# Kernel tuning notes

Hardware: AMD Instinct MI355X
Metric: run time of the kernel (lower is better)

## Reference

```python
import jax, jax.numpy as jnp
import numpy as np

B = 16384      # batch (original code uses B=1; break generalized per-sample)
H = 1024       # MLP hidden width from MLP([2, 1024, 1])
NMAX = 10      # RModel nmax default


def _mlp(x, W1, b1, W2, b2):
    # Linear(2->H) + ELU, then Linear(H->1) (no final activation: act=None)
    h = jax.nn.elu(x @ W1.T + b1)
    return h @ W2.T + b2


def setup_inputs() -> dict:
    key = jax.random.key(0)
    ks = jax.random.split(key, 5)
    X = jax.random.normal(ks[0], (B, 1), dtype=jnp.float32)
    Y = jnp.zeros((B, 1), dtype=jnp.float32)
    # _init_layers: Linear weights ~ N(0, 0.5), biases = 0
    de_W1 = 0.5 * jax.random.normal(ks[1], (H, 2), dtype=jnp.float32)
    de_b1 = jnp.zeros((H,), dtype=jnp.float32)
    de_W2 = 0.5 * jax.random.normal(ks[2], (1, H), dtype=jnp.float32)
    de_b2 = jnp.zeros((1,), dtype=jnp.float32)
    val_W1 = 0.5 * jax.random.normal(ks[3], (H, 2), dtype=jnp.float32)
    val_b1 = jnp.zeros((H,), dtype=jnp.float32)
    val_W2 = 0.5 * jax.random.normal(ks[4], (1, H), dtype=jnp.float32)
    val_b2 = jnp.zeros((1,), dtype=jnp.float32)
    return {"X": X, "Y": Y,
            "de_W1": de_W1, "de_b1": de_b1, "de_W2": de_W2, "de_b2": de_b2,
            "val_W1": val_W1, "val_b1": val_b1, "val_W2": val_W2, "val_b2": val_b2}


def reference(X, Y, de_W1, de_b1, de_W2, de_b2, val_W1, val_b1, val_W2, val_b2):
    # xen/yen are identity (defaults)
    xsig = X
    v0 = _mlp(jnp.concatenate([xsig, Y], axis=1), val_W1, val_b1, val_W2, val_b2)
    done0 = jnp.zeros((X.shape[0], 1), dtype=bool)

    def step(carry, i):
        y_prev, v_prev, done = carry
        y_new = y_prev + _mlp(jnp.concatenate([xsig, y_prev], axis=1),
                              de_W1, de_b1, de_W2, de_b2)
        v_new = _mlp(jnp.concatenate([xsig, y_new], axis=1),
                     val_W1, val_b1, val_W2, val_b2)
        # samples that already broke keep (freeze) their last appended (Y, V)
        y = jnp.where(done, y_prev, y_new)
        v = jnp.where(done, v_prev, v_new)
        # break condition: i > 0 and V >= previous V (appended first, then break)
        done = done | ((i > 0) & (v_new >= v_prev))
        return (y, v, done), (y, v)

    _, (ys, vs) = jax.lax.scan(step, (Y, v0, done0), jnp.arange(NMAX))
    y_stack = jnp.concatenate([Y[None], ys], axis=0)   # [NMAX+1, B, 1]
    v_stack = jnp.concatenate([v0[None], vs], axis=0)  # [NMAX+1, B, 1]
    return (y_stack, v_stack)
```

## Files before the change

kernel.cpp:

```cpp
#include <hip/hip_runtime.h>

#define NMAX 10
#define KPL  16
#define L2E  1.4426950408889634f
#define LN2  0.6931471805599453f

typedef float f2 __attribute__((ext_vector_type(2)));

template<int CTRL, int RMASK, int BMASK>
__device__ __forceinline__ float dppmov(float v) {
    return __int_as_float(__builtin_amdgcn_update_dpp(
        0, __float_as_int(v), CTRL, RMASK, BMASK, true));
}
__device__ __forceinline__ float rdlane63(float v) {
    return __int_as_float(__builtin_amdgcn_readlane(__float_as_int(v), 63));
}

__device__ __forceinline__ void wred2(float& a, float& b) {
    a += dppmov<0xB1, 0xf, 0xf>(a);  b += dppmov<0xB1, 0xf, 0xf>(b);
    a += dppmov<0x4E, 0xf, 0xf>(a);  b += dppmov<0x4E, 0xf, 0xf>(b);
    a += dppmov<0x141,0xf, 0xf>(a);  b += dppmov<0x141,0xf, 0xf>(b);
    a += dppmov<0x140,0xf, 0xf>(a);  b += dppmov<0x140,0xf, 0xf>(b);
    a += dppmov<0x142,0xa, 0xf>(a);  b += dppmov<0x142,0xa, 0xf>(b);
    a += dppmov<0x143,0xc, 0xf>(a);  b += dppmov<0x143,0xc, 0xf>(b);
    a = rdlane63(a);                 b = rdlane63(b);
}

__device__ __forceinline__ void mlp_joint(
    const float4* __restrict__ wl,
    const f2 (&u)[KPL],
    float y, float dbias, float vbias, float& dout, float& vout)
{
    const f2 yv   = {y, y};
    const f2 l2e  = {L2E, L2E};
    const f2 nl2e = {-L2E, -L2E};
    f2 acc0 = {0.f, 0.f}, acc1 = {0.f, 0.f};
#pragma unroll
    for (int k = 0; k < KPL; k += 2) {
        const float4 wa = wl[k * 64];
        const float4 wb = wl[(k + 1) * 64];
        f2 wya = {wa.x, wa.y}, w2a = {wa.z, wa.w};
        f2 wyb = {wb.x, wb.y}, w2b = {wb.z, wb.w};
        f2 p0 = __builtin_elementwise_fma(wya, yv, u[k]);
        f2 p1 = __builtin_elementwise_fma(wyb, yv, u[k + 1]);
        f2 e0, e1;
        e0.x = __builtin_amdgcn_exp2f(p0.x);  e0.y = __builtin_amdgcn_exp2f(p0.y);
        e1.x = __builtin_amdgcn_exp2f(p1.x);  e1.y = __builtin_amdgcn_exp2f(p1.y);
        f2 z0 = __builtin_elementwise_fma(e0, l2e, nl2e);
        f2 z1 = __builtin_elementwise_fma(e1, l2e, nl2e);
        f2 m0, m1;
        m0.x = __builtin_amdgcn_fmed3f(p0.x, z0.x, 0.f);
        m0.y = __builtin_amdgcn_fmed3f(p0.y, z0.y, 0.f);
        m1.x = __builtin_amdgcn_fmed3f(p1.x, z1.x, 0.f);
        m1.y = __builtin_amdgcn_fmed3f(p1.y, z1.y, 0.f);
        acc0 = __builtin_elementwise_fma(w2a, m0, acc0);
        acc1 = __builtin_elementwise_fma(w2b, m1, acc1);
    }
    float a = acc0.x + acc1.x;
    float b = acc0.y + acc1.y;
    wred2(a, b);
    dout = a + dbias; vout = b + vbias;
}

__global__ __launch_bounds__(256) void rmodel_kernel(
    const float* __restrict__ X, const float* __restrict__ Y,
    const float* __restrict__ de_W1, const float* __restrict__ de_b1,
    const float* __restrict__ de_W2, const float* __restrict__ de_b2,
    const float* __restrict__ val_W1, const float* __restrict__ val_b1,
    const float* __restrict__ val_W2, const float* __restrict__ val_b2,
    float* __restrict__ out, int n)
{
    __shared__ float4 wlds[KPL * 64];

    const int tid  = threadIdx.x;
    const int wid  = tid >> 6;
    const int lane = tid & 63;
    const int b    = blockIdx.x * 4 + wid;

#pragma unroll
    for (int i = 0; i < 4; ++i) {
        const int h = tid + i * 256;
        float2 w1d = reinterpret_cast<const float2*>(de_W1)[h];
        float2 w1v = reinterpret_cast<const float2*>(val_W1)[h];
        wlds[h] = make_float4(w1d.y * L2E, w1v.y * L2E,
                              de_W2[h] * LN2, val_W2[h] * LN2);
    }
    __syncthreads();

    if (b >= n) return;

    f2 u[KPL];
    const float x  = X[b];
    const float y0 = Y[b];
#pragma unroll
    for (int k = 0; k < KPL; ++k) {
        const int h = k * 64 + lane;
        float2 w1d = reinterpret_cast<const float2*>(de_W1)[h];
        float2 w1v = reinterpret_cast<const float2*>(val_W1)[h];
        u[k] = (f2){fmaf(w1d.x, x, de_b1[h]) * L2E,
                    fmaf(w1v.x, x, val_b1[h]) * L2E};
    }
    const float db2 = de_b2[0];
    const float vb2 = val_b2[0];
    const float4* wl = &wlds[lane];

    float* __restrict__ yout = out;
    float* __restrict__ vout = out + (size_t)(NMAX + 1) * n;

    float d, v;
    mlp_joint(wl, u, y0, db2, vb2, d, v);
    if (lane == 0) { yout[b] = y0; vout[b] = v; }

    float y     = y0 + d;
    float vprev = v;
    float yfin  = y0, vfin = v;
    int   kend  = NMAX;

    float* yp = yout + b;
    float* vp = vout + b;
    for (int k = 1; k <= NMAX; ++k) {
        yp += n; vp += n;
        float dk, vk;
        mlp_joint(wl, u, y, db2, vb2, dk, vk);
        if (lane == 0) { *yp = y; *vp = vk; }
        yfin = y; vfin = vk;
        if (k >= 2 && vk >= vprev) { kend = k; break; }
        vprev = vk;
        y += dk;
    }

    const int r = kend + 1 + lane;
    if (r <= NMAX) {
        yout[(size_t)r * n + b] = yfin;
        vout[(size_t)r * n + b] = vfin;
    }
}

extern "C" void kernel_launch(void* const* d_in, const int* in_sizes, int n_in,
                              void* d_out, int out_size, void* d_ws, size_t ws_size,
                              hipStream_t stream) {
    const float* X      = (const float*)d_in[0];
    const float* Y      = (const float*)d_in[1];
    const float* de_W1  = (const float*)d_in[2];
    const float* de_b1  = (const float*)d_in[3];
    const float* de_W2  = (const float*)d_in[4];
    const float* de_b2  = (const float*)d_in[5];
    const float* val_W1 = (const float*)d_in[6];
    const float* val_b1 = (const float*)d_in[7];
    const float* val_W2 = (const float*)d_in[8];
    const float* val_b2 = (const float*)d_in[9];
    float* out = (float*)d_out;

    const int n = in_sizes[0];
    dim3 block(256);
    dim3 grid((n + 3) / 4);
    hipLaunchKernelGGL(rmodel_kernel, grid, block, 0, stream,
                       X, Y, de_W1, de_b1, de_W2, de_b2,
                       val_W1, val_b1, val_W2, val_b2, out, n);
}
```

Before: 65.90 us.

## Process two samples per wavefront to share LDS weight loads and reductions

Each wavefront now handles a pair of samples, computing both MLP evaluations in one pass so every LDS weight float4 load serves two samples and the DPP cross-lane reductions are batched four-wide. When one sample breaks early, the other continues alone through a single-sample fallback loop. This adds register pressure (two sets of 16 precomputed u values) and halves the grid, and the per-step cost follows the slower sample of each pair.

```diff
diff --git a/kernel.cpp b/kernel.cpp
--- a/kernel.cpp
+++ b/kernel.cpp
@@ -16,50 +16,91 @@
     return __int_as_float(__builtin_amdgcn_readlane(__float_as_int(v), 63));
 }
 
+#define WRED_STAGE(CTRL, RM) \
+    a += dppmov<CTRL, RM, 0xf>(a);  b += dppmov<CTRL, RM, 0xf>(b);
+
 __device__ __forceinline__ void wred2(float& a, float& b) {
-    a += dppmov<0xB1, 0xf, 0xf>(a);  b += dppmov<0xB1, 0xf, 0xf>(b);
-    a += dppmov<0x4E, 0xf, 0xf>(a);  b += dppmov<0x4E, 0xf, 0xf>(b);
-    a += dppmov<0x141,0xf, 0xf>(a);  b += dppmov<0x141,0xf, 0xf>(b);
-    a += dppmov<0x140,0xf, 0xf>(a);  b += dppmov<0x140,0xf, 0xf>(b);
-    a += dppmov<0x142,0xa, 0xf>(a);  b += dppmov<0x142,0xa, 0xf>(b);
-    a += dppmov<0x143,0xc, 0xf>(a);  b += dppmov<0x143,0xc, 0xf>(b);
-    a = rdlane63(a);                 b = rdlane63(b);
+    WRED_STAGE(0xB1, 0xf)
+    WRED_STAGE(0x4E, 0xf)
+    WRED_STAGE(0x141,0xf)
+    WRED_STAGE(0x140,0xf)
+    WRED_STAGE(0x142,0xa)
+    WRED_STAGE(0x143,0xc)
+    a = rdlane63(a);  b = rdlane63(b);
+}
+
+#define WRED4_STAGE(CTRL, RM) \
+    a += dppmov<CTRL, RM, 0xf>(a);  b += dppmov<CTRL, RM, 0xf>(b); \
+    c += dppmov<CTRL, RM, 0xf>(c);  d += dppmov<CTRL, RM, 0xf>(d);
+
+__device__ __forceinline__ void wred4(float& a, float& b, float& c, float& d) {
+    WRED4_STAGE(0xB1, 0xf)
+    WRED4_STAGE(0x4E, 0xf)
+    WRED4_STAGE(0x141,0xf)
+    WRED4_STAGE(0x140,0xf)
+    WRED4_STAGE(0x142,0xa)
+    WRED4_STAGE(0x143,0xc)
+    a = rdlane63(a);  b = rdlane63(b);  c = rdlane63(c);  d = rdlane63(d);
+}
+
+__device__ __forceinline__ void unit_step(const float4 w, const f2 u, const f2 yv, f2& acc) {
+    const f2 l2e  = {L2E, L2E};
+    const f2 nl2e = {-L2E, -L2E};
+    f2 wy = {w.x, w.y}, w2 = {w.z, w.w};
+    f2 p = __builtin_elementwise_fma(wy, yv, u);
+    f2 e;
+    e.x = __builtin_amdgcn_exp2f(p.x);  e.y = __builtin_amdgcn_exp2f(p.y);
+    f2 z = __builtin_elementwise_fma(e, l2e, nl2e);
+    f2 m;
+    m.x = __builtin_amdgcn_fmed3f(p.x, z.x, 0.f);
+    m.y = __builtin_amdgcn_fmed3f(p.y, z.y, 0.f);
+    acc = __builtin_elementwise_fma(w2, m, acc);
 }
 
 __device__ __forceinline__ void mlp_joint(
-    const float4* __restrict__ wl,
-    const f2 (&u)[KPL],
+    const float4* __restrict__ wl, const f2 (&u)[KPL],
     float y, float dbias, float vbias, float& dout, float& vout)
 {
-    const f2 yv   = {y, y};
-    const f2 l2e  = {L2E, L2E};
-    const f2 nl2e = {-L2E, -L2E};
+    const f2 yv = {y, y};
     f2 acc0 = {0.f, 0.f}, acc1 = {0.f, 0.f};
 #pragma unroll
     for (int k = 0; k < KPL; k += 2) {
         const float4 wa = wl[k * 64];
         const float4 wb = wl[(k + 1) * 64];
-        f2 wya = {wa.x, wa.y}, w2a = {wa.z, wa.w};
-        f2 wyb = {wb.x, wb.y}, w2b = {wb.z, wb.w};
-        f2 p0 = __builtin_elementwise_fma(wya, yv, u[k]);
-        f2 p1 = __builtin_elementwise_fma(wyb, yv, u[k + 1]);
-        f2 e0, e1;
-        e0.x = __builtin_amdgcn_exp2f(p0.x);  e0.y = __builtin_amdgcn_exp2f(p0.y);
-        e1.x = __builtin_amdgcn_exp2f(p1.x);  e1.y = __builtin_amdgcn_exp2f(p1.y);
-        f2 z0 = __builtin_elementwise_fma(e0, l2e, nl2e);
-        f2 z1 = __builtin_elementwise_fma(e1, l2e, nl2e);
-        f2 m0, m1;
-        m0.x = __builtin_amdgcn_fmed3f(p0.x, z0.x, 0.f);
-        m0.y = __builtin_amdgcn_fmed3f(p0.y, z0.y, 0.f);
-        m1.x = __builtin_amdgcn_fmed3f(p1.x, z1.x, 0.f);
-        m1.y = __builtin_amdgcn_fmed3f(p1.y, z1.y, 0.f);
-        acc0 = __builtin_elementwise_fma(w2a, m0, acc0);
-        acc1 = __builtin_elementwise_fma(w2b, m1, acc1);
+        unit_step(wa, u[k],     yv, acc0);
+        unit_step(wb, u[k + 1], yv, acc1);
     }
     float a = acc0.x + acc1.x;
     float b = acc0.y + acc1.y;
     wred2(a, b);
     dout = a + dbias; vout = b + vbias;
+}
+
+__device__ __forceinline__ void mlp_joint2(
+    const float4* __restrict__ wl,
+    const f2 (&uA)[KPL], const f2 (&uB)[KPL],
+    float yA, float yB, float dbias, float vbias,
+    float& dA, float& vA, float& dB, float& vB)
+{
+    const f2 yvA = {yA, yA}, yvB = {yB, yB};
+    f2 aA0 = {0.f, 0.f}, aA1 = {0.f, 0.f};
+    f2 aB0 = {0.f, 0.f}, aB1 = {0.f, 0.f};
+#pragma unroll
+    for (int k = 0; k < KPL; k += 2) {
+        const float4 wa = wl[k * 64];
+        const float4 wb = wl[(k + 1) * 64];
+        unit_step(wa, uA[k],     yvA, aA0);
+        unit_step(wa, uB[k],     yvB, aB0);
+        unit_step(wb, uA[k + 1], yvA, aA1);
+        unit_step(wb, uB[k + 1], yvB, aB1);
+    }
+    float a = aA0.x + aA1.x;
+    float b = aA0.y + aA1.y;
+    float c = aB0.x + aB1.x;
+    float d = aB0.y + aB1.y;
+    wred4(a, b, c, d);
+    dA = a + dbias; vA = b + vbias;
+    dB = c + dbias; vB = d + vbias;
 }
 
 __global__ __launch_bounds__(256) void rmodel_kernel(
@@ -75,7 +116,6 @@
     const int tid  = threadIdx.x;
     const int wid  = tid >> 6;
     const int lane = tid & 63;
-    const int b    = blockIdx.x * 4 + wid;
 
 #pragma unroll
     for (int i = 0; i < 4; ++i) {
@@ -87,18 +127,23 @@
     }
     __syncthreads();
 
-    if (b >= n) return;
-
-    f2 u[KPL];
-    const float x  = X[b];
-    const float y0 = Y[b];
+    const int p  = blockIdx.x * 4 + wid;
+    const int bA = 2 * p;
+    if (bA >= n) return;
+    const bool hasB = (bA + 1 < n);
+    const int bB = hasB ? bA + 1 : bA;
+
+    f2 uA[KPL], uB[KPL];
+    const float xA = X[bA], xB = X[bB];
+    const float y0A = Y[bA], y0B = Y[bB];
 #pragma unroll
     for (int k = 0; k < KPL; ++k) {
         const int h = k * 64 + lane;
         float2 w1d = reinterpret_cast<const float2*>(de_W1)[h];
         float2 w1v = reinterpret_cast<const float2*>(val_W1)[h];
-        u[k] = (f2){fmaf(w1d.x, x, de_b1[h]) * L2E,
-                    fmaf(w1v.x, x, val_b1[h]) * L2E};
+        const float bd = de_b1[h], bv = val_b1[h];
+        uA[k] = (f2){fmaf(w1d.x, xA, bd) * L2E, fmaf(w1v.x, xA, bv) * L2E};
+        uB[k] = (f2){fmaf(w1d.x, xB, bd) * L2E, fmaf(w1v.x, xB, bv) * L2E};
     }
     const float db2 = de_b2[0];
     const float vb2 = val_b2[0];
@@ -107,32 +152,71 @@
     float* __restrict__ yout = out;
     float* __restrict__ vout = out + (size_t)(NMAX + 1) * n;
 
-    float d, v;
-    mlp_joint(wl, u, y0, db2, vb2, d, v);
-    if (lane == 0) { yout[b] = y0; vout[b] = v; }
-
-    float y     = y0 + d;
-    float vprev = v;
-    float yfin  = y0, vfin = v;
-    int   kend  = NMAX;
-
-    float* yp = yout + b;
-    float* vp = vout + b;
-    for (int k = 1; k <= NMAX; ++k) {
-        yp += n; vp += n;
+    float dA, vA, dB, vB;
+    mlp_joint2(wl, uA, uB, y0A, y0B, db2, vb2, dA, vA, dB, vB);
+    if (lane == 0) {
+        yout[bA] = y0A; vout[bA] = vA;
+        if (hasB) { yout[bB] = y0B; vout[bB] = vB; }
+    }
+
+    float yA = y0A + dA, yB = y0B + dB;
+    float vpA = vA, vpB = vB;
+    float yfinA = y0A, vfinA = vA, yfinB = y0B, vfinB = vB;
+    int kendA = NMAX, kendB = NMAX;
+    bool actA = true, actB = hasB;
+    int k = 1;
+
+    while (k <= NMAX && actA && actB) {
+        float dkA, vkA, dkB, vkB;
+        mlp_joint2(wl, uA, uB, yA, yB, db2, vb2, dkA, vkA, dkB, vkB);
+        if (lane == 0) {
+            yout[(size_t)k * n + bA] = yA; vout[(size_t)k * n + bA] = vkA;
+            yout[(size_t)k * n + bB] = yB; vout[(size_t)k * n + bB] = vkB;
+        }
+        yfinA = yA; vfinA = vkA; yfinB = yB; vfinB = vkB;
+        const bool brkA = (k >= 2) && (vkA >= vpA);
+        const bool brkB = (k >= 2) && (vkB >= vpB);
+        vpA = vkA; vpB = vkB;
+        if (brkA) { kendA = k; actA = false; } else { yA += dkA; }
+        if (brkB) { kendB = k; actB = false; } else { yB += dkB; }
+        ++k;
+    }
+    while (k <= NMAX && actA) {
         float dk, vk;
-        mlp_joint(wl, u, y, db2, vb2, dk, vk);
-        if (lane == 0) { *yp = y; *vp = vk; }
-        yfin = y; vfin = vk;
-        if (k >= 2 && vk >= vprev) { kend = k; break; }
-        vprev = vk;
-        y += dk;
-    }
-
-    const int r = kend + 1 + lane;
-    if (r <= NMAX) {
-        yout[(size_t)r * n + b] = yfin;
-        vout[(size_t)r * n + b] = vfin;
+        mlp_joint(wl, uA, yA, db2, vb2, dk, vk);
+        if (lane == 0) {
+            yout[(size_t)k * n + bA] = yA; vout[(size_t)k * n + bA] = vk;
+        }
+        yfinA = yA; vfinA = vk;
+        const bool brk = (k >= 2) && (vk >= vpA);
+        vpA = vk;
+        if (brk) { kendA = k; actA = false; } else { yA += dk; }
+        ++k;
+    }
+    while (k <= NMAX && actB) {
+        float dk, vk;
+        mlp_joint(wl, uB, yB, db2, vb2, dk, vk);
+        if (lane == 0) {
+            yout[(size_t)k * n + bB] = yB; vout[(size_t)k * n + bB] = vk;
+        }
+        yfinB = yB; vfinB = vk;
+        const bool brk = (k >= 2) && (vk >= vpB);
+        vpB = vk;
+        if (brk) { kendB = k; actB = false; } else { yB += dk; }
+        ++k;
+    }
+
+    const int rA = kendA + 1 + lane;
+    if (rA <= NMAX) {
+        yout[(size_t)rA * n + bA] = yfinA;
+        vout[(size_t)rA * n + bA] = vfinA;
+    }
+    if (hasB) {
+        const int rB = kendB + 1 + lane;
+        if (rB <= NMAX) {
+            yout[(size_t)rB * n + bB] = yfinB;
+            vout[(size_t)rB * n + bB] = vfinB;
+        }
     }
 }
 
@@ -151,9 +235,10 @@
     const float* val_b2 = (const float*)d_in[9];
     float* out = (float*)d_out;
 
-    const int n = in_sizes[0];
+    const int n     = in_sizes[0];
+    const int pairs = (n + 1) / 2;
     dim3 block(256);
-    dim3 grid((n + 3) / 4);
+    dim3 grid((pairs + 3) / 4);
     hipLaunchKernelGGL(rmodel_kernel, grid, block, 0, stream,
                        X, Y, de_W1, de_b1, de_W2, de_b2,
                        val_W1, val_b1, val_W2, val_b2, out, n);
```

Result: no change. 65.34 us (-0.9%).

## Split joint de/val MLP evaluation to skip unused final de network pass

Applied to the files above, without the earlier changes.

Evaluates the value and delta MLPs separately instead of jointly, so the delta network is only computed when its output will be used (not on the breaking or last iteration). The weight layout in shared memory is reorganized so each float4 packs two hidden units of one network. This removes wasted exp/FMA work but halves per-call instruction-level parallelism and doubles the number of cross-lane reductions.

```diff
diff --git a/kernel.cpp b/kernel.cpp
--- a/kernel.cpp
+++ b/kernel.cpp
@@ -1,7 +1,7 @@
 #include <hip/hip_runtime.h>
 
 #define NMAX 10
-#define KPL  16
+#define NP   8
 #define L2E  1.4426950408889634f
 #define LN2  0.6931471805599453f
 
@@ -16,50 +16,45 @@
     return __int_as_float(__builtin_amdgcn_readlane(__float_as_int(v), 63));
 }
 
-__device__ __forceinline__ void wred2(float& a, float& b) {
-    a += dppmov<0xB1, 0xf, 0xf>(a);  b += dppmov<0xB1, 0xf, 0xf>(b);
-    a += dppmov<0x4E, 0xf, 0xf>(a);  b += dppmov<0x4E, 0xf, 0xf>(b);
-    a += dppmov<0x141,0xf, 0xf>(a);  b += dppmov<0x141,0xf, 0xf>(b);
-    a += dppmov<0x140,0xf, 0xf>(a);  b += dppmov<0x140,0xf, 0xf>(b);
-    a += dppmov<0x142,0xa, 0xf>(a);  b += dppmov<0x142,0xa, 0xf>(b);
-    a += dppmov<0x143,0xc, 0xf>(a);  b += dppmov<0x143,0xc, 0xf>(b);
-    a = rdlane63(a);                 b = rdlane63(b);
+__device__ __forceinline__ float wred1(float a) {
+    a += dppmov<0xB1, 0xf, 0xf>(a);
+    a += dppmov<0x4E, 0xf, 0xf>(a);
+    a += dppmov<0x141,0xf, 0xf>(a);
+    a += dppmov<0x140,0xf, 0xf>(a);
+    a += dppmov<0x142,0xa, 0xf>(a);
+    a += dppmov<0x143,0xc, 0xf>(a);
+    return rdlane63(a);
 }
 
-__device__ __forceinline__ void mlp_joint(
-    const float4* __restrict__ wl,
-    const f2 (&u)[KPL],
-    float y, float dbias, float vbias, float& dout, float& vout)
-{
-    const f2 yv   = {y, y};
+__device__ __forceinline__ void unit_step(const f2 wy, const f2 w2,
+                                          const f2 u, const f2 yv, f2& acc) {
     const f2 l2e  = {L2E, L2E};
     const f2 nl2e = {-L2E, -L2E};
+    f2 p = __builtin_elementwise_fma(wy, yv, u);
+    f2 e;
+    e.x = __builtin_amdgcn_exp2f(p.x);  e.y = __builtin_amdgcn_exp2f(p.y);
+    f2 z = __builtin_elementwise_fma(e, l2e, nl2e);
+    f2 m;
+    m.x = __builtin_amdgcn_fmed3f(p.x, z.x, 0.f);
+    m.y = __builtin_amdgcn_fmed3f(p.y, z.y, 0.f);
+    acc = __builtin_elementwise_fma(w2, m, acc);
+}
+
+__device__ __forceinline__ float mlp_one(
+    const float4* __restrict__ wl,
+    const f2 (&u)[NP], float y, float bias)
+{
+    const f2 yv = {y, y};
     f2 acc0 = {0.f, 0.f}, acc1 = {0.f, 0.f};
 #pragma unroll
-    for (int k = 0; k < KPL; k += 2) {
-        const float4 wa = wl[k * 64];
-        const float4 wb = wl[(k + 1) * 64];
-        f2 wya = {wa.x, wa.y}, w2a = {wa.z, wa.w};
-        f2 wyb = {wb.x, wb.y}, w2b = {wb.z, wb.w};
-        f2 p0 = __builtin_elementwise_fma(wya, yv, u[k]);
-        f2 p1 = __builtin_elementwise_fma(wyb, yv, u[k + 1]);
-        f2 e0, e1;
-        e0.x = __builtin_amdgcn_exp2f(p0.x);  e0.y = __builtin_amdgcn_exp2f(p0.y);
-        e1.x = __builtin_amdgcn_exp2f(p1.x);  e1.y = __builtin_amdgcn_exp2f(p1.y);
-        f2 z0 = __builtin_elementwise_fma(e0, l2e, nl2e);
-        f2 z1 = __builtin_elementwise_fma(e1, l2e, nl2e);
-        f2 m0, m1;
-        m0.x = __builtin_amdgcn_fmed3f(p0.x, z0.x, 0.f);
-        m0.y = __builtin_amdgcn_fmed3f(p0.y, z0.y, 0.f);
-        m1.x = __builtin_amdgcn_fmed3f(p1.x, z1.x, 0.f);
-        m1.y = __builtin_amdgcn_fmed3f(p1.y, z1.y, 0.f);
-        acc0 = __builtin_elementwise_fma(w2a, m0, acc0);
-        acc1 = __builtin_elementwise_fma(w2b, m1, acc1);
+    for (int p = 0; p < NP; p += 2) {
+        const float4 wa = wl[p * 64];
+        const float4 wb = wl[(p + 1) * 64];
+        unit_step((f2){wa.x, wa.y}, (f2){wa.z, wa.w}, u[p],     yv, acc0);
+        unit_step((f2){wb.x, wb.y}, (f2){wb.z, wb.w}, u[p + 1], yv, acc1);
     }
-    float a = acc0.x + acc1.x;
-    float b = acc0.y + acc1.y;
-    wred2(a, b);
-    dout = a + dbias; vout = b + vbias;
+    f2 acc = acc0 + acc1;
+    return wred1(acc.x + acc.y) + bias;
 }
 
 __global__ __launch_bounds__(256) void rmodel_kernel(
@@ -70,48 +65,52 @@
     const float* __restrict__ val_W2, const float* __restrict__ val_b2,
     float* __restrict__ out, int n)
 {
-    __shared__ float4 wlds[KPL * 64];
+    __shared__ float4 wlds[2 * NP * 64];
 
     const int tid  = threadIdx.x;
     const int wid  = tid >> 6;
     const int lane = tid & 63;
-    const int b    = blockIdx.x * 4 + wid;
 
 #pragma unroll
     for (int i = 0; i < 4; ++i) {
-        const int h = tid + i * 256;
-        float2 w1d = reinterpret_cast<const float2*>(de_W1)[h];
-        float2 w1v = reinterpret_cast<const float2*>(val_W1)[h];
-        wlds[h] = make_float4(w1d.y * L2E, w1v.y * L2E,
-                              de_W2[h] * LN2, val_W2[h] * LN2);
+        const int e  = tid + i * 256;
+        const int a  = e >> 9;
+        const int ei = e & 511;
+        const int p  = ei >> 6, l = ei & 63;
+        const int h0 = l + (p << 7), h1 = h0 + 64;
+        const float* W1 = a ? de_W1 : val_W1;
+        const float* W2 = a ? de_W2 : val_W2;
+        wlds[e] = make_float4(W1[2 * h0 + 1] * L2E, W1[2 * h1 + 1] * L2E,
+                              W2[h0] * LN2,         W2[h1] * LN2);
     }
     __syncthreads();
 
+    const int b = blockIdx.x * 4 + wid;
     if (b >= n) return;
 
-    f2 u[KPL];
+    f2 uv[NP], ud[NP];
     const float x  = X[b];
     const float y0 = Y[b];
 #pragma unroll
-    for (int k = 0; k < KPL; ++k) {
-        const int h = k * 64 + lane;
-        float2 w1d = reinterpret_cast<const float2*>(de_W1)[h];
-        float2 w1v = reinterpret_cast<const float2*>(val_W1)[h];
-        u[k] = (f2){fmaf(w1d.x, x, de_b1[h]) * L2E,
-                    fmaf(w1v.x, x, val_b1[h]) * L2E};
+    for (int p = 0; p < NP; ++p) {
+        const int h0 = lane + (p << 7), h1 = h0 + 64;
+        uv[p] = (f2){fmaf(val_W1[2 * h0], x, val_b1[h0]) * L2E,
+                     fmaf(val_W1[2 * h1], x, val_b1[h1]) * L2E};
+        ud[p] = (f2){fmaf(de_W1[2 * h0], x, de_b1[h0]) * L2E,
+                     fmaf(de_W1[2 * h1], x, de_b1[h1]) * L2E};
     }
     const float db2 = de_b2[0];
     const float vb2 = val_b2[0];
-    const float4* wl = &wlds[lane];
+    const float4* wlv = &wlds[lane];
+    const float4* wld = &wlds[512 + lane];
 
     float* __restrict__ yout = out;
     float* __restrict__ vout = out + (size_t)(NMAX + 1) * n;
 
-    float d, v;
-    mlp_joint(wl, u, y0, db2, vb2, d, v);
+    float v = mlp_one(wlv, uv, y0, vb2);
     if (lane == 0) { yout[b] = y0; vout[b] = v; }
 
-    float y     = y0 + d;
+    float y     = y0 + mlp_one(wld, ud, y0, db2);
     float vprev = v;
     float yfin  = y0, vfin = v;
     int   kend  = NMAX;
@@ -120,13 +119,12 @@
     float* vp = vout + b;
     for (int k = 1; k <= NMAX; ++k) {
         yp += n; vp += n;
-        float dk, vk;
-        mlp_joint(wl, u, y, db2, vb2, dk, vk);
+        const float vk = mlp_one(wlv, uv, y, vb2);
         if (lane == 0) { *yp = y; *vp = vk; }
         yfin = y; vfin = vk;
         if (k >= 2 && vk >= vprev) { kend = k; break; }
         vprev = vk;
-        y += dk;
+        if (k < NMAX) y += mlp_one(wld, ud, y, db2);
     }
 
     const int r = kend + 1 + lane;
```

Result: no change. 64.98 us (median of 3 runs) (-1.4%).
